# Kernel optimization log

Measured on AMD Instinct MI355X. Metric: run time of the kernel, lower is better.

Reference implementation:

```python
import jax, jax.numpy as jnp
import numpy as np
import math

T_STEPS = 100      # diffusion steps
TED = 16           # time_embed_dim
NODE_C = 4         # node_num_classes
EDGE_C = 2         # edge_num_classes
HID = 64           # hidden_dim
H = 4              # nhead
B = 256            # graphs per batch
NPG = 64           # nodes per graph
DEG = 8            # avg out-degree
N = B * NPG
E = N * DEG
IN_CH = NODE_C + TED  # 20


def sinusoidal_embedding(t_vec, dim):
    # t_vec: [1] float. Matches get_sinusoidal_embedding for even dim.
    half = dim // 2
    scale = math.log(10000.0) / (half - 1)
    freqs = jnp.exp(-jnp.arange(half, dtype=jnp.float32) * scale)  # [half]
    emb = t_vec[:, None] * freqs[None, :]                          # [1, half]
    return jnp.concatenate([jnp.sin(emb), jnp.cos(emb)], axis=1)   # [1, dim]


def transformer_conv(x, src, dst, Wq, bq, Wk, bk, Wv, bv, Ws, bs):
    # PyG TransformerConv, concat=False (mean over heads), root_weight=True,
    # beta=False, no edge features, dropout=0 (eval).
    n = x.shape[0]
    q = (x @ Wq + bq).reshape(n, H, HID)
    k = (x @ Wk + bk).reshape(n, H, HID)
    v = (x @ Wv + bv).reshape(n, H, HID)
    # attention logits per edge, softmax over incoming edges of each dst node
    logits = jnp.sum(q[dst] * k[src], axis=-1) / math.sqrt(HID)    # [E, H]
    lmax = jax.ops.segment_max(logits, dst, num_segments=n)       # [n, H]
    ex = jnp.exp(logits - lmax[dst])                              # [E, H]
    denom = jax.ops.segment_sum(ex, dst, num_segments=n)          # [n, H]
    attn = ex / jnp.where(denom == 0, 1.0, denom)[dst]            # [E, H]
    msg = v[src] * attn[:, :, None]                               # [E, H, HID]
    agg = jax.ops.segment_sum(msg, dst, num_segments=n)           # [n, H, HID]
    return agg.mean(axis=1) + x @ Ws + bs                         # [n, HID]


def setup_inputs() -> dict:
    key = jax.random.key(0)
    ks = jax.random.split(key, 32)

    # node features: random one-hot labels
    labels = jax.random.randint(ks[0], (N,), 0, NODE_C)
    x = jax.nn.one_hot(labels, NODE_C, dtype=jnp.float32)

    # per-graph random edges (kept within each graph via offsets)
    src_l = jax.random.randint(ks[1], (B, NPG * DEG), 0, NPG)
    dst_l = jax.random.randint(ks[2], (B, NPG * DEG), 0, NPG)
    off = (jnp.arange(B) * NPG)[:, None]
    edge_index = jnp.stack([(src_l + off).reshape(-1), (dst_l + off).reshape(-1)]).astype(jnp.int64)

    batch = jnp.repeat(jnp.arange(B, dtype=jnp.int64), NPG)

    def lin(k, fin, fout):
        kw, kb = jax.random.split(k)
        W = jax.random.normal(kw, (fin, fout), jnp.float32) / math.sqrt(fin)
        b = jax.random.normal(kb, (fout,), jnp.float32) * 0.01
        return W, b

    W_time, b_time = lin(ks[3], TED, TED)
    Wq1, bq1 = lin(ks[4], IN_CH, H * HID)
    Wk1, bk1 = lin(ks[5], IN_CH, H * HID)
    Wv1, bv1 = lin(ks[6], IN_CH, H * HID)
    Ws1, bs1 = lin(ks[7], IN_CH, HID)
    Wq2, bq2 = lin(ks[8], HID, H * HID)
    Wk2, bk2 = lin(ks[9], HID, H * HID)
    Wv2, bv2 = lin(ks[10], HID, H * HID)
    Ws2, bs2 = lin(ks[11], HID, HID)
    W_node, b_node = lin(ks[12], HID, NODE_C)
    W_e1, b_e1 = lin(ks[13], 2 * HID, HID)
    W_e2, b_e2 = lin(ks[14], HID, EDGE_C)

    return dict(x=x, edge_index=edge_index, batch=batch, t=50,
                W_time=W_time, b_time=b_time,
                Wq1=Wq1, bq1=bq1, Wk1=Wk1, bk1=bk1, Wv1=Wv1, bv1=bv1, Ws1=Ws1, bs1=bs1,
                Wq2=Wq2, bq2=bq2, Wk2=Wk2, bk2=bk2, Wv2=Wv2, bv2=bv2, Ws2=Ws2, bs2=bs2,
                W_node=W_node, b_node=b_node, W_e1=W_e1, b_e1=b_e1, W_e2=W_e2, b_e2=b_e2)


def reference(x, edge_index, batch, t,
              W_time, b_time,
              Wq1, bq1, Wk1, bk1, Wv1, bv1, Ws1, bs1,
              Wq2, bq2, Wk2, bk2, Wv2, bv2, Ws2, bs2,
              W_node, b_node, W_e1, b_e1, W_e2, b_e2):
    src, dst = edge_index[0], edge_index[1]

    # time embedding: sinusoidal(t/T) -> Linear -> broadcast to all nodes
    t_vec = jnp.asarray([t], jnp.float32) / T_STEPS
    temb = sinusoidal_embedding(t_vec, TED) @ W_time + b_time      # [1, TED]
    temb = jnp.broadcast_to(temb, (x.shape[0], TED))
    x_in = jnp.concatenate([x, temb], axis=1)                      # [N, 20]

    h = jax.nn.relu(transformer_conv(x_in, src, dst, Wq1, bq1, Wk1, bk1, Wv1, bv1, Ws1, bs1))
    h = jax.nn.relu(transformer_conv(h, src, dst, Wq2, bq2, Wk2, bk2, Wv2, bv2, Ws2, bs2))

    node_logits = h @ W_node + b_node                              # [N, 4]

    # to_dense_batch with equal-sized graphs == reshape; vectorized edge MLP
    hd = h.reshape(B, NPG, HID)
    pair = jnp.concatenate([
        jnp.broadcast_to(hd[:, :, None, :], (B, NPG, NPG, HID)),
        jnp.broadcast_to(hd[:, None, :, :], (B, NPG, NPG, HID)),
    ], axis=-1)                                                    # [B, n, n, 2*HID]
    e_hidden = jax.nn.relu(pair @ W_e1 + b_e1)
    edge_logits = e_hidden @ W_e2 + b_e2                           # [B, n, n, 2]
    return node_logits, edge_logits
```

## Files before the change

kernel.cpp:

```cpp
#include <hip/hip_runtime.h>
#include <math.h>

constexpr int EPG  = 512;
constexpr int ETOT = 131072;

constexpr size_t TAB_Q  = 0;
constexpr size_t TAB_K  = 1024;
constexpr size_t TAB_V  = 2048;
constexpr size_t TAB_S  = 3072;
constexpr size_t TAB_LG = 3328;
constexpr size_t OFF_H2P = 65536;

constexpr int PK_V_HI   = 0;
constexpr int PK_V_LO   = 16384;
constexpr int PK_S_HI   = 32768;
constexpr int PK_S_LO   = 36864;
constexpr int PK_E1T_HI = 40960;
constexpr int PK_E1T_LO = 45056;
constexpr int PK_E1B_HI = 49152;
constexpr int PK_E1B_LO = 53248;
constexpr int PK_M_HI   = 57344;
constexpr int PK_M_LO   = 73728;
constexpr int PK_VV_HI  = 90112;
constexpr int PK_VV_LO  = 91136;
constexpr int PK_N_HI   = 92160;
constexpr int PK_N_LO   = 93184;

typedef short bf16x8 __attribute__((ext_vector_type(8)));
typedef float f32x4  __attribute__((ext_vector_type(4)));

__device__ __forceinline__ short f2bf(float x) {
    unsigned u = __float_as_uint(x);
    u = (u + 0x7fffu + ((u >> 16) & 1u)) >> 16;
    return (short)u;
}
__device__ __forceinline__ float bf2f(short h) {
    return __uint_as_float(((unsigned)(unsigned short)h) << 16);
}
__device__ __forceinline__ void splt(float x, short& hi, short& lo) {
    hi = f2bf(x);
    lo = f2bf(x - bf2f(hi));
}
__device__ __forceinline__ unsigned packsplt(float x) {
    short hi, lo; splt(x, hi, lo);
    return ((unsigned)(unsigned short)hi << 16) | (unsigned short)lo;
}

__device__ __forceinline__ f32x4 mfma3(bf16x8 ah, bf16x8 al, bf16x8 bh, bf16x8 bl, f32x4 c) {
    c = __builtin_amdgcn_mfma_f32_16x16x32_bf16(ah, bh, c, 0, 0, 0);
    c = __builtin_amdgcn_mfma_f32_16x16x32_bf16(ah, bl, c, 0, 0, 0);
    c = __builtin_amdgcn_mfma_f32_16x16x32_bf16(al, bh, c, 0, 0, 0);
    return c;
}

__device__ __forceinline__ bf16x8 ldsfrag(const short* p, int rowb, int kb, int lane) {
    return *(const bf16x8*)&p[(rowb + (lane & 15)) * 72 + kb + ((lane >> 4) << 3)];
}
__device__ __forceinline__ bf16x8 gpfrag(const short* p, int colb, int kb, int lane) {
    return *(const bf16x8*)&p[((colb + (lane & 15)) << 6) + kb + ((lane >> 4) << 3)];
}
__device__ __forceinline__ void unpack8(const unsigned* p, bf16x8& hv, bf16x8& lv) {
    uint4 a = *(const uint4*)p;
    uint4 b = *(const uint4*)(p + 4);
    unsigned u[8] = {a.x, a.y, a.z, a.w, b.x, b.y, b.z, b.w};
    bf16x8 h, l;
    #pragma unroll
    for (int i = 0; i < 8; i++) { h[i] = (short)(u[i] >> 16); l[i] = (short)(u[i] & 0xffffu); }
    hv = h; lv = l;
}

__global__ __launch_bounds__(256) void k_tabprep(
    const int* __restrict__ t_ptr,
    const float* __restrict__ Wt,  const float* __restrict__ bt,
    const float* __restrict__ Wq1, const float* __restrict__ bq1,
    const float* __restrict__ Wk1, const float* __restrict__ bk1,
    const float* __restrict__ Wv1, const float* __restrict__ bv1,
    const float* __restrict__ Ws1, const float* __restrict__ bs1,
    const float* __restrict__ Wq2, const float* __restrict__ bq2,
    const float* __restrict__ Wk2, const float* __restrict__ Wv2,
    const float* __restrict__ Ws2, const float* __restrict__ We1,
    const float* __restrict__ Wn,
    float* __restrict__ ws, short* __restrict__ wsh)
{
    const int t = threadIdx.x, b = blockIdx.x;
    if (b < 112) {
        const float* src; int N; int dhi; int nb;
        if (b < 64)      { src = Wv2;           N = 256; dhi = PK_V_HI;   nb = b; }
        else if (b < 80) { src = Ws2;           N = 64;  dhi = PK_S_HI;   nb = b - 64; }
        else if (b < 96) { src = We1;           N = 64;  dhi = PK_E1T_HI; nb = b - 80; }
        else             { src = We1 + 64 * 64; N = 64;  dhi = PK_E1B_HI; nb = b - 96; }
        int dlo = dhi + N * 64;
        int n = nb * 4 + (t >> 6), kk = t & 63;
        float v = src[(size_t)kk * N + n];
        short hi, lo; splt(v, hi, lo);
        wsh[dhi + n * 64 + kk] = hi;
        wsh[dlo + n * 64 + kk] = lo;
        return;
    }
    if (b < 128) {
        int h = (b - 112) >> 2, m0 = ((b - 112) & 3) * 16;
        __shared__ __align__(16) float wq[64][68];
        __shared__ __align__(16) float wk[16][68];
        for (int i = t; i < 1024; i += 256) {
            int r = i >> 4, c4 = (i & 15) * 4;
            *(float4*)&wq[r][c4] = *(const float4*)&Wq2[(size_t)r * 256 + h * 64 + c4];
        }
        {
            int r = t >> 4, c4 = (t & 15) * 4;
            *(float4*)&wk[r][c4] = *(const float4*)&Wk2[(size_t)(m0 + r) * 256 + h * 64 + c4];
        }
        __syncthreads();
        const int m = m0 + (t >> 4), kk0 = (t & 15) * 4;
        const float* wkr = &wk[t >> 4][0];
        for (int kk = kk0; kk < kk0 + 4; kk++) {
            const float* wqr = &wq[kk][0];
            float acc = 0.f;
            #pragma unroll
            for (int a = 0; a < 64; a += 4) {
                float4 qa = *(const float4*)(wqr + a);
                float4 ka = *(const float4*)(wkr + a);
                acc += qa.x * ka.x + qa.y * ka.y + qa.z * ka.z + qa.w * ka.w;
            }
            acc *= 0.125f;
            short hi, lo; splt(acc, hi, lo);
            wsh[PK_M_HI + h * 4096 + m * 64 + kk] = hi;
            wsh[PK_M_LO + h * 4096 + m * 64 + kk] = lo;
        }
        return;
    }
    if (b < 132) {
        int h = b - 128;
        if (t < 64) {
            float acc = 0.f;
            for (int a = 0; a < 64; a++)
                acc += Wk2[(size_t)t * 256 + h * 64 + a] * bq2[h * 64 + a];
            short hi, lo; splt(0.125f * acc, hi, lo);
            wsh[PK_VV_HI + h * 64 + t] = hi;
            wsh[PK_VV_LO + h * 64 + t] = lo;
        }
        return;
    }
    __shared__ float se[16], temb[16];
    __shared__ float q1t[4][256], k1t[4][256], v1t[4][256], s1t[4][64];
    if (t < 8) {
        float tv = (float)(*t_ptr) * 0.01f;
        float scale = logf(10000.0f) / 7.0f;
        float e = tv * expf(-(float)t * scale);
        se[t]     = sinf(e);
        se[t + 8] = cosf(e);
    }
    __syncthreads();
    if (t < 16) {
        float acc = bt[t];
        for (int i = 0; i < 16; i++) acc += se[i] * Wt[i * 16 + t];
        temb[t] = acc;
    }
    __syncthreads();
    {
        const int o = t;
        float tq = 0.f, tk = 0.f, tv = 0.f;
        for (int d = 0; d < 16; d++) {
            float td = temb[d];
            tq += td * Wq1[(4 + d) * 256 + o];
            tk += td * Wk1[(4 + d) * 256 + o];
            tv += td * Wv1[(4 + d) * 256 + o];
        }
        for (int c = 0; c < 4; c++) {
            q1t[c][o] = Wq1[c * 256 + o] + tq + bq1[o];
            k1t[c][o] = Wk1[c * 256 + o] + tk + bk1[o];
            v1t[c][o] = Wv1[c * 256 + o] + tv + bv1[o];
        }
        if (o < 64) {
            float ts = 0.f;
            for (int d = 0; d < 16; d++) ts += temb[d] * Ws1[(4 + d) * 64 + o];
            for (int c = 0; c < 4; c++) s1t[c][o] = Ws1[c * 64 + o] + ts + bs1[o];
        }
    }
    __syncthreads();
    for (int idx = t; idx < 1024; idx += 256) {
        int c = idx >> 8, o = idx & 255;
        ws[TAB_Q + idx] = q1t[c][o];
        ws[TAB_K + idx] = k1t[c][o];
        ws[TAB_V + idx] = v1t[c][o];
    }
    ws[TAB_S + t] = s1t[t >> 6][t & 63];
    if (t < 64) {
        int cd = t >> 4, cs = (t >> 2) & 3, h = t & 3;
        float acc = 0.f;
        for (int d = 0; d < 64; d++) acc += q1t[cd][h * 64 + d] * k1t[cs][h * 64 + d];
        ws[TAB_LG + t] = acc * 0.125f;
    }
    for (int idx = t; idx < 1024; idx += 256) {
        int c = idx >> 6, k = idx & 63;
        float v = (c < 4) ? Wn[k * 4 + c] : 0.f;
        short hi, lo; splt(v, hi, lo);
        wsh[PK_N_HI + idx] = hi;
        wsh[PK_N_LO + idx] = lo;
    }
    for (int idx = 256 + t; idx < 1024; idx += 256) {
        wsh[PK_VV_HI + idx] = 0;
        wsh[PK_VV_LO + idx] = 0;
    }
}

__global__ __launch_bounds__(256) void k_main(
    const float* __restrict__ x, const int* __restrict__ ei,
    const float* __restrict__ ws, const short* __restrict__ wsh,
    const float* __restrict__ bv, const float* __restrict__ bsk,
    unsigned* __restrict__ h2p)
{
    __shared__ __align__(16) char smem[77376];
    short* hHi = (short*)(smem);
    short* hLo = (short*)(smem + 9216);
    short* tHi = (short*)(smem + 18432);
    short* tLo = (short*)(smem + 27648);
    char*  R1base = smem + 36864;
    char*  R2base = smem + 55296;
    char*  Cc     = smem + 73728;
    float* wcolb  = (float*)(smem + 74816);
    float* lgs    = (float*)(smem + 75840);
    int*   cls    = (int*)(smem + 76096);
    int*   cnt4   = (int*)(smem + 76352);
    float* v1t    = (float*)(smem + 36864);
    float* s1t    = (float*)(smem + 40960);

    const int g    = blockIdx.x >> 2;
    const int i0   = (blockIdx.x & 3) * 16;
    const int t    = threadIdx.x;
    const int lane = t & 63, w = t >> 6;
    const int lg4  = ((lane >> 4) << 2);
    const int lg8  = ((lane >> 4) << 3);
    const int l15  = lane & 15;

    short* GHi = (short*)(R1base + w * 4608);
    short* GLo = (short*)(R1base + w * 4608 + 2304);
    float* Sf  = (float*)(R2base + w * 4608);

    for (int i = t; i < 1024; i += 256) v1t[i] = ws[TAB_V + i];
    s1t[t] = ws[TAB_S + t];
    if (t < 64)  lgs[t] = ws[TAB_LG + t];
    if (t < 64) {
        const float* xr = x + (size_t)(g * 64 + t) * 4;
        int c = 0;
        if (xr[1] > 0.5f) c = 1;
        if (xr[2] > 0.5f) c = 2;
        if (xr[3] > 0.5f) c = 3;
        cls[t] = c;
    }
    cnt4[t] = 0;
    for (int i = t; i < 272; i += 256) ((int*)Cc)[i] = 0;
    __syncthreads();

    for (int e = t; e < EPG; e += 256) {
        int ge = g * EPG + e;
        int ls = ei[ge] - g * 64;
        int ld = ei[ETOT + ge] - g * 64;
        atomicAdd(&cnt4[ld * 4 + cls[ls]], 1);
        int lr = ld - i0;
        if ((unsigned)lr < 16u) {
            int idx = lr * 68 + ls;
            atomicAdd((int*)(Cc + (idx & ~3)), 1 << ((idx & 3) * 8));
        }
    }
    __syncthreads();

    {
        const int row = t >> 2, d0 = (t & 3) * 16;
        int cd = cls[row];
        int c0 = cnt4[row * 4], c1 = cnt4[row * 4 + 1],
            c2 = cnt4[row * 4 + 2], c3 = cnt4[row * 4 + 3];
        float a[16];
        #pragma unroll
        for (int hh = 0; hh < 4; hh++) {
            float l0 = lgs[cd * 16 + hh], l1 = lgs[cd * 16 + 4 + hh],
                  l2 = lgs[cd * 16 + 8 + hh], l3 = lgs[cd * 16 + 12 + hh];
            float m = -1e30f;
            if (c0 > 0) m = fmaxf(m, l0);
            if (c1 > 0) m = fmaxf(m, l1);
            if (c2 > 0) m = fmaxf(m, l2);
            if (c3 > 0) m = fmaxf(m, l3);
            float e0 = (c0 > 0) ? (float)c0 * __expf(l0 - m) : 0.f;
            float e1 = (c1 > 0) ? (float)c1 * __expf(l1 - m) : 0.f;
            float e2 = (c2 > 0) ? (float)c2 * __expf(l2 - m) : 0.f;
            float e3 = (c3 > 0) ? (float)c3 * __expf(l3 - m) : 0.f;
            float den = e0 + e1 + e2 + e3;
            float inv = (den > 0.f) ? 0.25f / den : 0.f;
            a[hh * 4 + 0] = e0 * inv; a[hh * 4 + 1] = e1 * inv;
            a[hh * 4 + 2] = e2 * inv; a[hh * 4 + 3] = e3 * inv;
        }
        bf16x8 vh0, vl0, vh1, vl1;
        #pragma unroll
        for (int jj = 0; jj < 16; jj++) {
            int d = d0 + jj;
            float acc = s1t[cd * 64 + d];
            #pragma unroll
            for (int hh = 0; hh < 4; hh++)
                #pragma unroll
                for (int c = 0; c < 4; c++)
                    acc += a[hh * 4 + c] * v1t[c * 256 + hh * 64 + d];
            float o = fmaxf(acc, 0.f);
            short hi, lo; splt(o, hi, lo);
            if (jj < 8) { vh0[jj] = hi; vl0[jj] = lo; }
            else        { vh1[jj - 8] = hi; vl1[jj - 8] = lo; }
            tHi[d * 72 + row] = hi;
            tLo[d * 72 + row] = lo;
        }
        *(bf16x8*)&hHi[row * 72 + d0]     = vh0;
        *(bf16x8*)&hLo[row * 72 + d0]     = vl0;
        *(bf16x8*)&hHi[row * 72 + d0 + 8] = vh1;
        *(bf16x8*)&hLo[row * 72 + d0 + 8] = vl1;
    }
    __syncthreads();

    const int h = w;

    bf16x8 AhQ0 = ldsfrag(hHi, i0, 0, lane),  AhQ1 = ldsfrag(hHi, i0, 32, lane);
    bf16x8 AlQ0 = ldsfrag(hLo, i0, 0, lane),  AlQ1 = ldsfrag(hLo, i0, 32, lane);

    f32x4 skacc = {0.f, 0.f, 0.f, 0.f};
    {
        int cb = w * 16;
        skacc = mfma3(AhQ0, AlQ0, gpfrag(wsh + PK_S_HI, cb, 0, lane),
                                   gpfrag(wsh + PK_S_LO, cb, 0, lane), skacc);
        skacc = mfma3(AhQ1, AlQ1, gpfrag(wsh + PK_S_HI, cb, 32, lane),
                                   gpfrag(wsh + PK_S_LO, cb, 32, lane), skacc);
        float bb = bsk[cb + l15];
        #pragma unroll
        for (int r = 0; r < 4; r++) skacc[r] += bb;
    }

    {
        bf16x8 vv0h = gpfrag(wsh + PK_VV_HI, 0, 0, lane);
        bf16x8 vv0l = gpfrag(wsh + PK_VV_LO, 0, 0, lane);
        bf16x8 vv1h = gpfrag(wsh + PK_VV_HI, 0, 32, lane);
        bf16x8 vv1l = gpfrag(wsh + PK_VV_LO, 0, 32, lane);
        #pragma unroll
        for (int jb = 0; jb < 64; jb += 16) {
            f32x4 wc = {0.f, 0.f, 0.f, 0.f};
            wc = mfma3(ldsfrag(hHi, jb, 0, lane),  ldsfrag(hLo, jb, 0, lane),  vv0h, vv0l, wc);
            wc = mfma3(ldsfrag(hHi, jb, 32, lane), ldsfrag(hLo, jb, 32, lane), vv1h, vv1l, wc);
            if (l15 == h) {
                #pragma unroll
                for (int r = 0; r < 4; r++) wcolb[h * 64 + jb + lg4 + r] = wc[r];
            }
        }
    }

    {
        const short* pmh = wsh + PK_M_HI + h * 4096;
        const short* pml = wsh + PK_M_LO + h * 4096;
        #pragma unroll
        for (int mb = 0; mb < 64; mb += 16) {
            f32x4 ga = {0.f, 0.f, 0.f, 0.f};
            ga = mfma3(AhQ0, AlQ0, gpfrag(pmh, mb, 0, lane),  gpfrag(pml, mb, 0, lane),  ga);
            ga = mfma3(AhQ1, AlQ1, gpfrag(pmh, mb, 32, lane), gpfrag(pml, mb, 32, lane), ga);
            #pragma unroll
            for (int r = 0; r < 4; r++) {
                short hi, lo; splt(ga[r], hi, lo);
                GHi[(lg4 + r) * 72 + mb + l15] = hi;
                GLo[(lg4 + r) * 72 + mb + l15] = lo;
            }
        }
    }

    {
        bf16x8 g0h = ldsfrag(GHi, 0, 0, lane),  g0l = ldsfrag(GLo, 0, 0, lane);
        bf16x8 g1h = ldsfrag(GHi, 0, 32, lane), g1l = ldsfrag(GLo, 0, 32, lane);
        #pragma unroll
        for (int jb = 0; jb < 64; jb += 16) {
            f32x4 s = {0.f, 0.f, 0.f, 0.f};
            s = mfma3(g0h, g0l, ldsfrag(hHi, jb, 0, lane),  ldsfrag(hLo, jb, 0, lane),  s);
            s = mfma3(g1h, g1l, ldsfrag(hHi, jb, 32, lane), ldsfrag(hLo, jb, 32, lane), s);
            #pragma unroll
            for (int r = 0; r < 4; r++)
                Sf[(lg4 + r) * 68 + jb + l15] = s[r];
        }
    }

    bf16x8 pa0h, pa0l, pa1h, pa1l;
    {
        const int lr = l15;
        float sv[16];
        {
            const float* sp = Sf + lr * 68;
            float4 a0 = *(const float4*)(sp + lg8);
            float4 a1 = *(const float4*)(sp + lg8 + 4);
            float4 a2 = *(const float4*)(sp + 32 + lg8);
            float4 a3 = *(const float4*)(sp + 32 + lg8 + 4);
            sv[0]=a0.x; sv[1]=a0.y; sv[2]=a0.z; sv[3]=a0.w;
            sv[4]=a1.x; sv[5]=a1.y; sv[6]=a1.z; sv[7]=a1.w;
            sv[8]=a2.x; sv[9]=a2.y; sv[10]=a2.z; sv[11]=a2.w;
            sv[12]=a3.x; sv[13]=a3.y; sv[14]=a3.z; sv[15]=a3.w;
        }
        int cv[16];
        {
            const unsigned* crow = (const unsigned*)(Cc + lr * 68);
            unsigned c0 = crow[lg8 >> 2], c1 = crow[(lg8 >> 2) + 1];
            unsigned c2 = crow[(32 + lg8) >> 2], c3 = crow[((32 + lg8) >> 2) + 1];
            #pragma unroll
            for (int e = 0; e < 4; e++) {
                cv[e]      = (c0 >> (e * 8)) & 255;
                cv[4 + e]  = (c1 >> (e * 8)) & 255;
                cv[8 + e]  = (c2 >> (e * 8)) & 255;
                cv[12 + e] = (c3 >> (e * 8)) & 255;
            }
        }
        #pragma unroll
        for (int e = 0; e < 8; e++) {
            sv[e]     += wcolb[h * 64 + lg8 + e];
            sv[8 + e] += wcolb[h * 64 + 32 + lg8 + e];
        }
        float m = -1e30f;
        #pragma unroll
        for (int e = 0; e < 16; e++) if (cv[e] > 0) m = fmaxf(m, sv[e]);
        m = fmaxf(m, __shfl_xor(m, 16));
        m = fmaxf(m, __shfl_xor(m, 32));
        float den = 0.f; float p[16];
        #pragma unroll
        for (int e = 0; e < 16; e++) {
            p[e] = (cv[e] > 0) ? (float)cv[e] * __expf(sv[e] - m) : 0.f;
            den += p[e];
        }
        den += __shfl_xor(den, 16);
        den += __shfl_xor(den, 32);
        float inv = (den > 0.f) ? 1.f / den : 0.f;
        #pragma unroll
        for (int e = 0; e < 8; e++) {
            short hi, lo;
            splt(p[e] * inv, hi, lo);      pa0h[e] = hi; pa0l[e] = lo;
            splt(p[8 + e] * inv, hi, lo);  pa1h[e] = hi; pa1l[e] = lo;
        }
    }

    #pragma unroll
    for (int fb = 0; fb < 64; fb += 16) {
        f32x4 u = {0.f, 0.f, 0.f, 0.f};
        u = mfma3(pa0h, pa0l, ldsfrag(tHi, fb, 0, lane),  ldsfrag(tLo, fb, 0, lane),  u);
        u = mfma3(pa1h, pa1l, ldsfrag(tHi, fb, 32, lane), ldsfrag(tLo, fb, 32, lane), u);
        #pragma unroll
        for (int r = 0; r < 4; r++) {
            short hi, lo; splt(u[r], hi, lo);
            GHi[(lg4 + r) * 72 + fb + l15] = hi;
            GLo[(lg4 + r) * 72 + fb + l15] = lo;
        }
    }

    {
        bf16x8 u0h = ldsfrag(GHi, 0, 0, lane),  u0l = ldsfrag(GLo, 0, 0, lane);
        bf16x8 u1h = ldsfrag(GHi, 0, 32, lane), u1l = ldsfrag(GLo, 0, 32, lane);
        #pragma unroll
        for (int db = 0; db < 64; db += 16) {
            int gc = h * 64 + db;
            f32x4 pv = {0.f, 0.f, 0.f, 0.f};
            pv = mfma3(u0h, u0l, gpfrag(wsh + PK_V_HI, gc, 0, lane),
                                  gpfrag(wsh + PK_V_LO, gc, 0, lane), pv);
            pv = mfma3(u1h, u1l, gpfrag(wsh + PK_V_HI, gc, 32, lane),
                                  gpfrag(wsh + PK_V_LO, gc, 32, lane), pv);
            #pragma unroll
            for (int r = 0; r < 4; r++)
                Sf[(lg4 + r) * 68 + db + l15] = pv[r];
        }
    }
    __syncthreads();

    {
        const int d = w * 16 + l15;
        float bvsum = bv[d] + bv[64 + d] + bv[128 + d] + bv[192 + d];
        #pragma unroll
        for (int r = 0; r < 4; r++) {
            float sum = 0.f;
            #pragma unroll
            for (int hh = 0; hh < 4; hh++)
                sum += ((const float*)(R2base + hh * 4608))[(lg4 + r) * 68 + d];
            float v = fmaxf(0.25f * (sum + bvsum) + skacc[r], 0.f);
            h2p[(size_t)(g * 64 + i0 + lg4 + r) * 64 + d] = packsplt(v);
        }
    }
}

__global__ __launch_bounds__(256) void k_edge(
    const short* __restrict__ wsh, const unsigned* __restrict__ h2g,
    const float* __restrict__ bn, const float* __restrict__ be1,
    const float* __restrict__ We2, const float* __restrict__ be2,
    float* __restrict__ out)
{
    __shared__ __align__(16) char smem[39680];
    unsigned* h2P = (unsigned*)(smem);
    float*    Af  = (float*)(smem + 17408);
    float*    BTf = (float*)(smem + 21760);
    float*    w2s = (float*)(smem + 39168);

    const int g  = blockIdx.x >> 2;
    const int i0 = (blockIdx.x & 3) * 16;
    const int t  = threadIdx.x;
    const int lane = t & 63, w = t >> 6;
    const int lg4 = ((lane >> 4) << 2);
    const int lg8 = ((lane >> 4) << 3);
    const int l15 = lane & 15;

    {
        int row = t >> 2, c16 = (t & 3) * 16;
        const unsigned* src = h2g + (size_t)(g * 64 + row) * 64 + c16;
        #pragma unroll
        for (int q = 0; q < 4; q++)
            *(uint4*)&h2P[row * 68 + c16 + q * 4] = *(const uint4*)(src + q * 4);
    }
    if (t < 128) w2s[(t & 1) * 64 + (t >> 1)] = We2[t];
    __syncthreads();

    {
        bf16x8 aq0, lq0, aq1, lq1;
        const unsigned* ap = h2P + (i0 + l15) * 68;
        unpack8(ap + lg8, aq0, lq0);
        unpack8(ap + 32 + lg8, aq1, lq1);
        {
            int colb = w * 16;
            bf16x8 e0h = gpfrag(wsh + PK_E1T_HI, colb, 0, lane),  e0l = gpfrag(wsh + PK_E1T_LO, colb, 0, lane);
            bf16x8 e1h = gpfrag(wsh + PK_E1T_HI, colb, 32, lane), e1l = gpfrag(wsh + PK_E1T_LO, colb, 32, lane);
            f32x4 aa = {0.f, 0.f, 0.f, 0.f};
            aa = mfma3(aq0, lq0, e0h, e0l, aa);
            aa = mfma3(aq1, lq1, e1h, e1l, aa);
            float bev = be1[colb + l15];
            #pragma unroll
            for (int r = 0; r < 4; r++)
                Af[(lg4 + r) * 68 + colb + l15] = aa[r] + bev;
        }
        if (w == 0) {
            bf16x8 n0h = gpfrag(wsh + PK_N_HI, 0, 0, lane),  n0l = gpfrag(wsh + PK_N_LO, 0, 0, lane);
            bf16x8 n1h = gpfrag(wsh + PK_N_HI, 0, 32, lane), n1l = gpfrag(wsh + PK_N_LO, 0, 32, lane);
            f32x4 nl = {0.f, 0.f, 0.f, 0.f};
            nl = mfma3(aq0, lq0, n0h, n0l, nl);
            nl = mfma3(aq1, lq1, n1h, n1l, nl);
            if (l15 < 4) {
                #pragma unroll
                for (int r = 0; r < 4; r++)
                    out[(size_t)(g * 64 + i0 + lg4 + r) * 4 + l15] = nl[r] + bn[l15];
            }
        }
    }
    {
        bf16x8 af0, lf0, af1, lf1;
        const unsigned* ap = h2P + (w * 16 + l15) * 68;
        unpack8(ap + lg8, af0, lf0);
        unpack8(ap + 32 + lg8, af1, lf1);
        #pragma unroll
        for (int ct = 0; ct < 4; ct++) {
            int colb = ct * 16;
            bf16x8 b0h = gpfrag(wsh + PK_E1B_HI, colb, 0, lane),  b0l = gpfrag(wsh + PK_E1B_LO, colb, 0, lane);
            bf16x8 b1h = gpfrag(wsh + PK_E1B_HI, colb, 32, lane), b1l = gpfrag(wsh + PK_E1B_LO, colb, 32, lane);
            f32x4 bb = {0.f, 0.f, 0.f, 0.f};
            bb = mfma3(af0, lf0, b0h, b0l, bb);
            bb = mfma3(af1, lf1, b1h, b1l, bb);
            #pragma unroll
            for (int r = 0; r < 4; r++)
                BTf[(colb + l15) * 68 + w * 16 + lg4 + r] = bb[r];
        }
    }
    __syncthreads();

    {
        const int j = t & 63;
        float e0[4], e1[4];
        const float cb0 = be2[0], cb1 = be2[1];
        #pragma unroll
        for (int ii = 0; ii < 4; ii++) { e0[ii] = cb0; e1[ii] = cb1; }
        for (int kb = 0; kb < 4; kb++) {
            const int k0 = kb * 16;
            float bj[16], wa[16], wb[16];
            #pragma unroll
            for (int q = 0; q < 16; q++) {
                bj[q] = BTf[(k0 + q) * 68 + j];
                wa[q] = w2s[k0 + q];
                wb[q] = w2s[64 + k0 + q];
            }
            #pragma unroll
            for (int ii = 0; ii < 4; ii++) {
                const float* ar = &Af[(w * 4 + ii) * 68 + k0];
                #pragma unroll
                for (int q = 0; q < 16; q += 4) {
                    float4 a4 = *(const float4*)(ar + q);
                    float s;
                    s = fmaxf(a4.x + bj[q + 0], 0.f); e0[ii] += s * wa[q + 0]; e1[ii] += s * wb[q + 0];
                    s = fmaxf(a4.y + bj[q + 1], 0.f); e0[ii] += s * wa[q + 1]; e1[ii] += s * wb[q + 1];
                    s = fmaxf(a4.z + bj[q + 2], 0.f); e0[ii] += s * wa[q + 2]; e1[ii] += s * wb[q + 2];
                    s = fmaxf(a4.w + bj[q + 3], 0.f); e0[ii] += s * wa[q + 3]; e1[ii] += s * wb[q + 3];
                }
            }
        }
        float2* oe = (float2*)(out + 65536);
        #pragma unroll
        for (int ii = 0; ii < 4; ii++)
            oe[(size_t)(g * 64 + i0 + w * 4 + ii) * 64 + j] = make_float2(e0[ii], e1[ii]);
    }
}

extern "C" void kernel_launch(void* const* d_in, const int* in_sizes, int n_in,
                              void* d_out, int out_size, void* d_ws, size_t ws_size,
                              hipStream_t stream)
{
    const float* x    = (const float*)d_in[0];
    const int*   ei   = (const int*)d_in[1];
    const int*   tptr = (const int*)d_in[3];
    const float* Wt   = (const float*)d_in[4];
    const float* bt   = (const float*)d_in[5];
    const float* Wq1  = (const float*)d_in[6];
    const float* bq1  = (const float*)d_in[7];
    const float* Wk1  = (const float*)d_in[8];
    const float* bk1  = (const float*)d_in[9];
    const float* Wv1  = (const float*)d_in[10];
    const float* bv1  = (const float*)d_in[11];
    const float* Ws1  = (const float*)d_in[12];
    const float* bs1  = (const float*)d_in[13];
    const float* Wq2  = (const float*)d_in[14];
    const float* bq2  = (const float*)d_in[15];
    const float* Wk2  = (const float*)d_in[16];
    const float* Wv2  = (const float*)d_in[18];
    const float* bv2  = (const float*)d_in[19];
    const float* Ws2  = (const float*)d_in[20];
    const float* bs2  = (const float*)d_in[21];
    const float* Wn   = (const float*)d_in[22];
    const float* bn   = (const float*)d_in[23];
    const float* We1  = (const float*)d_in[24];
    const float* be1  = (const float*)d_in[25];
    const float* We2  = (const float*)d_in[26];
    const float* be2  = (const float*)d_in[27];

    float* ws  = (float*)d_ws;
    short* wsh = (short*)(ws + 4096);
    unsigned* h2p = (unsigned*)(ws + OFF_H2P);
    float* out = (float*)d_out;

    k_tabprep<<<133, 256, 0, stream>>>(tptr, Wt, bt, Wq1, bq1, Wk1, bk1, Wv1, bv1,
                                       Ws1, bs1, Wq2, bq2, Wk2, Wv2, Ws2, We1, Wn,
                                       ws, wsh);
    k_main<<<1024, 256, 0, stream>>>(x, ei, ws, wsh, bv2, bs2, h2p);
    k_edge<<<1024, 256, 0, stream>>>(wsh, h2p, bn, be1, We2, be2, out);
}
```

Measured before the change: 64.02 us.

## Split layer-1 computation into separate kernel to avoid 4x redundant recompute

Layer-1 node features, their transposed copy and the per-head column term were previously recomputed by each of the four blocks handling a graph. A new k_h1 kernel (one block per graph) now computes them once and writes packed hi/lo bf16 pairs to global memory. k_main reads those fragments from global memory instead of LDS, which shrinks its shared-memory footprint and can raise occupancy. The cost is an extra kernel launch plus global round-trips for h1, its transpose and wcol, and MFMA operands are now unpacked from global loads.

```diff
diff --git a/kernel.cpp b/kernel.cpp
--- a/kernel.cpp
+++ b/kernel.cpp
@@ -9,7 +9,10 @@
 constexpr size_t TAB_V  = 2048;
 constexpr size_t TAB_S  = 3072;
 constexpr size_t TAB_LG = 3328;
-constexpr size_t OFF_H2P = 65536;
+constexpr size_t OFF_H2P  = 65536;
+constexpr size_t OFF_H1P  = 1114112;
+constexpr size_t OFF_H1TP = 2162688;
+constexpr size_t OFF_WCOL = 3211264;
 
 constexpr int PK_V_HI   = 0;
 constexpr int PK_V_LO   = 16384;
@@ -53,9 +56,6 @@
     return c;
 }
 
-__device__ __forceinline__ bf16x8 ldsfrag(const short* p, int rowb, int kb, int lane) {
-    return *(const bf16x8*)&p[(rowb + (lane & 15)) * 72 + kb + ((lane >> 4) << 3)];
-}
 __device__ __forceinline__ bf16x8 gpfrag(const short* p, int colb, int kb, int lane) {
     return *(const bf16x8*)&p[((colb + (lane & 15)) << 6) + kb + ((lane >> 4) << 3)];
 }
@@ -67,6 +67,10 @@
     #pragma unroll
     for (int i = 0; i < 8; i++) { h[i] = (short)(u[i] >> 16); l[i] = (short)(u[i] & 0xffffu); }
     hv = h; lv = l;
+}
+__device__ __forceinline__ void pkfrag(const unsigned* p, int rowb, int kb, int stride,
+                                       int lane, bf16x8& hv, bf16x8& lv) {
+    unpack8(p + (size_t)(rowb + (lane & 15)) * stride + kb + ((lane >> 4) << 3), hv, lv);
 }
 
 __global__ __launch_bounds__(256) void k_tabprep(
@@ -203,42 +207,25 @@
     }
 }
 
-__global__ __launch_bounds__(256) void k_main(
+__global__ __launch_bounds__(256) void k_h1(
     const float* __restrict__ x, const int* __restrict__ ei,
     const float* __restrict__ ws, const short* __restrict__ wsh,
-    const float* __restrict__ bv, const float* __restrict__ bsk,
-    unsigned* __restrict__ h2p)
+    unsigned* __restrict__ h1p, unsigned* __restrict__ h1tp,
+    float* __restrict__ wcolg)
 {
-    __shared__ __align__(16) char smem[77376];
-    short* hHi = (short*)(smem);
-    short* hLo = (short*)(smem + 9216);
-    short* tHi = (short*)(smem + 18432);
-    short* tLo = (short*)(smem + 27648);
-    char*  R1base = smem + 36864;
-    char*  R2base = smem + 55296;
-    char*  Cc     = smem + 73728;
-    float* wcolb  = (float*)(smem + 74816);
-    float* lgs    = (float*)(smem + 75840);
-    int*   cls    = (int*)(smem + 76096);
-    int*   cnt4   = (int*)(smem + 76352);
-    float* v1t    = (float*)(smem + 36864);
-    float* s1t    = (float*)(smem + 40960);
-
-    const int g    = blockIdx.x >> 2;
-    const int i0   = (blockIdx.x & 3) * 16;
-    const int t    = threadIdx.x;
-    const int lane = t & 63, w = t >> 6;
-    const int lg4  = ((lane >> 4) << 2);
-    const int lg8  = ((lane >> 4) << 3);
-    const int l15  = lane & 15;
-
-    short* GHi = (short*)(R1base + w * 4608);
-    short* GLo = (short*)(R1base + w * 4608 + 2304);
-    float* Sf  = (float*)(R2base + w * 4608);
+    __shared__ float v1t[1024];
+    __shared__ float s1t[256];
+    __shared__ float lgs[64];
+    __shared__ float vvf[256];
+    __shared__ int   cls[64];
+    __shared__ int   cnt4[256];
+
+    const int g = blockIdx.x, t = threadIdx.x;
 
     for (int i = t; i < 1024; i += 256) v1t[i] = ws[TAB_V + i];
     s1t[t] = ws[TAB_S + t];
-    if (t < 64)  lgs[t] = ws[TAB_LG + t];
+    if (t < 64) lgs[t] = ws[TAB_LG + t];
+    vvf[t] = bf2f(wsh[PK_VV_HI + t]) + bf2f(wsh[PK_VV_LO + t]);
     if (t < 64) {
         const float* xr = x + (size_t)(g * 64 + t) * 4;
         int c = 0;
@@ -248,7 +235,6 @@
         cls[t] = c;
     }
     cnt4[t] = 0;
-    for (int i = t; i < 272; i += 256) ((int*)Cc)[i] = 0;
     __syncthreads();
 
     for (int e = t; e < EPG; e += 256) {
@@ -256,11 +242,6 @@
         int ls = ei[ge] - g * 64;
         int ld = ei[ETOT + ge] - g * 64;
         atomicAdd(&cnt4[ld * 4 + cls[ls]], 1);
-        int lr = ld - i0;
-        if ((unsigned)lr < 16u) {
-            int idx = lr * 68 + ls;
-            atomicAdd((int*)(Cc + (idx & ~3)), 1 << ((idx & 3) * 8));
-        }
     }
     __syncthreads();
 
@@ -288,7 +269,8 @@
             a[hh * 4 + 0] = e0 * inv; a[hh * 4 + 1] = e1 * inv;
             a[hh * 4 + 2] = e2 * inv; a[hh * 4 + 3] = e3 * inv;
         }
-        bf16x8 vh0, vl0, vh1, vl1;
+        float h1v[16];
+        unsigned pk[16];
         #pragma unroll
         for (int jj = 0; jj < 16; jj++) {
             int d = d0 + jj;
@@ -299,23 +281,81 @@
                 for (int c = 0; c < 4; c++)
                     acc += a[hh * 4 + c] * v1t[c * 256 + hh * 64 + d];
             float o = fmaxf(acc, 0.f);
-            short hi, lo; splt(o, hi, lo);
-            if (jj < 8) { vh0[jj] = hi; vl0[jj] = lo; }
-            else        { vh1[jj - 8] = hi; vl1[jj - 8] = lo; }
-            tHi[d * 72 + row] = hi;
-            tLo[d * 72 + row] = lo;
-        }
-        *(bf16x8*)&hHi[row * 72 + d0]     = vh0;
-        *(bf16x8*)&hLo[row * 72 + d0]     = vl0;
-        *(bf16x8*)&hHi[row * 72 + d0 + 8] = vh1;
-        *(bf16x8*)&hLo[row * 72 + d0 + 8] = vl1;
-    }
-    __syncthreads();
-
-    const int h = w;
-
-    bf16x8 AhQ0 = ldsfrag(hHi, i0, 0, lane),  AhQ1 = ldsfrag(hHi, i0, 32, lane);
-    bf16x8 AlQ0 = ldsfrag(hLo, i0, 0, lane),  AlQ1 = ldsfrag(hLo, i0, 32, lane);
+            h1v[jj] = o;
+            pk[jj] = packsplt(o);
+        }
+        unsigned* dst = h1p + ((size_t)(g * 64 + row) << 6) + d0;
+        *(uint4*)(dst)      = make_uint4(pk[0], pk[1], pk[2], pk[3]);
+        *(uint4*)(dst + 4)  = make_uint4(pk[4], pk[5], pk[6], pk[7]);
+        *(uint4*)(dst + 8)  = make_uint4(pk[8], pk[9], pk[10], pk[11]);
+        *(uint4*)(dst + 12) = make_uint4(pk[12], pk[13], pk[14], pk[15]);
+        unsigned* tb = h1tp + (size_t)g * 4096;
+        #pragma unroll
+        for (int jj = 0; jj < 16; jj++) tb[(d0 + jj) * 64 + row] = pk[jj];
+        float ph[4];
+        #pragma unroll
+        for (int hh = 0; hh < 4; hh++) {
+            float acc = 0.f;
+            #pragma unroll
+            for (int jj = 0; jj < 16; jj++) acc += h1v[jj] * vvf[hh * 64 + d0 + jj];
+            ph[hh] = acc;
+        }
+        #pragma unroll
+        for (int hh = 0; hh < 4; hh++) {
+            ph[hh] += __shfl_xor(ph[hh], 1);
+            ph[hh] += __shfl_xor(ph[hh], 2);
+        }
+        int hsel = t & 3;
+        wcolg[(size_t)g * 256 + hsel * 64 + row] = ph[hsel];
+    }
+}
+
+__global__ __launch_bounds__(256) void k_main(
+    const int* __restrict__ ei, const short* __restrict__ wsh,
+    const unsigned* __restrict__ h1p, const unsigned* __restrict__ h1tp,
+    const float* __restrict__ wcolg,
+    const float* __restrict__ bv, const float* __restrict__ bsk,
+    unsigned* __restrict__ h2p)
+{
+    __shared__ __align__(16) char smem[36928];
+    char*  R1 = smem;
+    char*  R2 = smem + 17408;
+    char*  Cc = smem + 34816;
+    float* wcolS = (float*)(smem + 35904);
+
+    const int g    = blockIdx.x >> 2;
+    const int i0   = (blockIdx.x & 3) * 16;
+    const int t    = threadIdx.x;
+    const int lane = t & 63, w = t >> 6;
+    const int lg4  = ((lane >> 4) << 2);
+    const int lg8  = ((lane >> 4) << 3);
+    const int l15  = lane & 15;
+    const int h    = w;
+
+    unsigned* Gp  = (unsigned*)(R1 + w * 4352);
+    float*    Sf  = (float*)(R2 + w * 4352);
+    unsigned* Up  = (unsigned*)(R2 + w * 4352);
+
+    wcolS[t] = wcolg[(size_t)g * 256 + t];
+    for (int i = t; i < 272; i += 256) ((int*)Cc)[i] = 0;
+    __syncthreads();
+
+    for (int e = t; e < EPG; e += 256) {
+        int ge = g * EPG + e;
+        int ls = ei[ge] - g * 64;
+        int ld = ei[ETOT + ge] - g * 64;
+        int lr = ld - i0;
+        if ((unsigned)lr < 16u) {
+            int idx = lr * 68 + ls;
+            atomicAdd((int*)(Cc + (idx & ~3)), 1 << ((idx & 3) * 8));
+        }
+    }
+    __syncthreads();
+
+    const unsigned* h1g = h1p + ((size_t)g << 12);
+    bf16x8 AhQ0, AlQ0, AhQ1, AlQ1;
+    pkfrag(h1g, i0, 0, 64, lane, AhQ0, AlQ0);
+    pkfrag(h1g, i0, 32, 64, lane, AhQ1, AlQ1);
 
     f32x4 skacc = {0.f, 0.f, 0.f, 0.f};
     {
@@ -330,23 +370,6 @@
     }
 
     {
-        bf16x8 vv0h = gpfrag(wsh + PK_VV_HI, 0, 0, lane);
-        bf16x8 vv0l = gpfrag(wsh + PK_VV_LO, 0, 0, lane);
-        bf16x8 vv1h = gpfrag(wsh + PK_VV_HI, 0, 32, lane);
-        bf16x8 vv1l = gpfrag(wsh + PK_VV_LO, 0, 32, lane);
-        #pragma unroll
-        for (int jb = 0; jb < 64; jb += 16) {
-            f32x4 wc = {0.f, 0.f, 0.f, 0.f};
-            wc = mfma3(ldsfrag(hHi, jb, 0, lane),  ldsfrag(hLo, jb, 0, lane),  vv0h, vv0l, wc);
-            wc = mfma3(ldsfrag(hHi, jb, 32, lane), ldsfrag(hLo, jb, 32, lane), vv1h, vv1l, wc);
-            if (l15 == h) {
-                #pragma unroll
-                for (int r = 0; r < 4; r++) wcolb[h * 64 + jb + lg4 + r] = wc[r];
-            }
-        }
-    }
-
-    {
         const short* pmh = wsh + PK_M_HI + h * 4096;
         const short* pml = wsh + PK_M_LO + h * 4096;
         #pragma unroll
@@ -355,29 +378,29 @@
             ga = mfma3(AhQ0, AlQ0, gpfrag(pmh, mb, 0, lane),  gpfrag(pml, mb, 0, lane),  ga);
             ga = mfma3(AhQ1, AlQ1, gpfrag(pmh, mb, 32, lane), gpfrag(pml, mb, 32, lane), ga);
             #pragma unroll
-            for (int r = 0; r < 4; r++) {
-                short hi, lo; splt(ga[r], hi, lo);
-                GHi[(lg4 + r) * 72 + mb + l15] = hi;
-                GLo[(lg4 + r) * 72 + mb + l15] = lo;
-            }
-        }
-    }
-
-    {
-        bf16x8 g0h = ldsfrag(GHi, 0, 0, lane),  g0l = ldsfrag(GLo, 0, 0, lane);
-        bf16x8 g1h = ldsfrag(GHi, 0, 32, lane), g1l = ldsfrag(GLo, 0, 32, lane);
+            for (int r = 0; r < 4; r++)
+                Gp[(lg4 + r) * 68 + mb + l15] = packsplt(ga[r]);
+        }
+    }
+
+    {
+        bf16x8 g0h, g0l, g1h, g1l;
+        pkfrag(Gp, 0, 0, 68, lane, g0h, g0l);
+        pkfrag(Gp, 0, 32, 68, lane, g1h, g1l);
         #pragma unroll
         for (int jb = 0; jb < 64; jb += 16) {
+            bf16x8 b0h, b0l, b1h, b1l;
+            pkfrag(h1g, jb, 0, 64, lane, b0h, b0l);
+            pkfrag(h1g, jb, 32, 64, lane, b1h, b1l);
             f32x4 s = {0.f, 0.f, 0.f, 0.f};
-            s = mfma3(g0h, g0l, ldsfrag(hHi, jb, 0, lane),  ldsfrag(hLo, jb, 0, lane),  s);
-            s = mfma3(g1h, g1l, ldsfrag(hHi, jb, 32, lane), ldsfrag(hLo, jb, 32, lane), s);
+            s = mfma3(g0h, g0l, b0h, b0l, s);
+            s = mfma3(g1h, g1l, b1h, b1l, s);
             #pragma unroll
             for (int r = 0; r < 4; r++)
                 Sf[(lg4 + r) * 68 + jb + l15] = s[r];
         }
     }
 
-    bf16x8 pa0h, pa0l, pa1h, pa1l;
     {
         const int lr = l15;
         float sv[16];
@@ -407,8 +430,8 @@
         }
         #pragma unroll
         for (int e = 0; e < 8; e++) {
-            sv[e]     += wcolb[h * 64 + lg8 + e];
-            sv[8 + e] += wcolb[h * 64 + 32 + lg8 + e];
+            sv[e]     += wcolS[h * 64 + lg8 + e];
+            sv[8 + e] += wcolS[h * 64 + 32 + lg8 + e];
         }
         float m = -1e30f;
         #pragma unroll
@@ -424,30 +447,40 @@
         den += __shfl_xor(den, 16);
         den += __shfl_xor(den, 32);
         float inv = (den > 0.f) ? 1.f / den : 0.f;
-        #pragma unroll
-        for (int e = 0; e < 8; e++) {
-            short hi, lo;
-            splt(p[e] * inv, hi, lo);      pa0h[e] = hi; pa0l[e] = lo;
-            splt(p[8 + e] * inv, hi, lo);  pa1h[e] = hi; pa1l[e] = lo;
-        }
-    }
-
-    #pragma unroll
-    for (int fb = 0; fb < 64; fb += 16) {
-        f32x4 u = {0.f, 0.f, 0.f, 0.f};
-        u = mfma3(pa0h, pa0l, ldsfrag(tHi, fb, 0, lane),  ldsfrag(tLo, fb, 0, lane),  u);
-        u = mfma3(pa1h, pa1l, ldsfrag(tHi, fb, 32, lane), ldsfrag(tLo, fb, 32, lane), u);
-        #pragma unroll
-        for (int r = 0; r < 4; r++) {
-            short hi, lo; splt(u[r], hi, lo);
-            GHi[(lg4 + r) * 72 + fb + l15] = hi;
-            GLo[(lg4 + r) * 72 + fb + l15] = lo;
-        }
-    }
-
-    {
-        bf16x8 u0h = ldsfrag(GHi, 0, 0, lane),  u0l = ldsfrag(GLo, 0, 0, lane);
-        bf16x8 u1h = ldsfrag(GHi, 0, 32, lane), u1l = ldsfrag(GLo, 0, 32, lane);
+        unsigned pk[16];
+        #pragma unroll
+        for (int e = 0; e < 16; e++) pk[e] = packsplt(p[e] * inv);
+        unsigned* pp = Gp + lr * 68;
+        *(uint4*)(pp + lg8)          = make_uint4(pk[0], pk[1], pk[2], pk[3]);
+        *(uint4*)(pp + lg8 + 4)      = make_uint4(pk[4], pk[5], pk[6], pk[7]);
+        *(uint4*)(pp + 32 + lg8)     = make_uint4(pk[8], pk[9], pk[10], pk[11]);
+        *(uint4*)(pp + 32 + lg8 + 4) = make_uint4(pk[12], pk[13], pk[14], pk[15]);
+    }
+
+    {
+        bf16x8 p0h, p0l, p1h, p1l;
+        pkfrag(Gp, 0, 0, 68, lane, p0h, p0l);
+        pkfrag(Gp, 0, 32, 68, lane, p1h, p1l);
+        const unsigned* tg = h1tp + ((size_t)g << 12);
+        #pragma unroll
+        for (int fb = 0; fb < 64; fb += 16) {
+            bf16x8 b0h, b0l, b1h, b1l;
+            pkfrag(tg, fb, 0, 64, lane, b0h, b0l);
+            pkfrag(tg, fb, 32, 64, lane, b1h, b1l);
+            f32x4 u = {0.f, 0.f, 0.f, 0.f};
+            u = mfma3(p0h, p0l, b0h, b0l, u);
+            u = mfma3(p1h, p1l, b1h, b1l, u);
+            #pragma unroll
+            for (int r = 0; r < 4; r++)
+                Up[(lg4 + r) * 68 + fb + l15] = packsplt(u[r]);
+        }
+    }
+
+    {
+        bf16x8 u0h, u0l, u1h, u1l;
+        pkfrag(Up, 0, 0, 68, lane, u0h, u0l);
+        pkfrag(Up, 0, 32, 68, lane, u1h, u1l);
+        float* PVf = (float*)Gp;
         #pragma unroll
         for (int db = 0; db < 64; db += 16) {
             int gc = h * 64 + db;
@@ -458,7 +491,7 @@
                                   gpfrag(wsh + PK_V_LO, gc, 32, lane), pv);
             #pragma unroll
             for (int r = 0; r < 4; r++)
-                Sf[(lg4 + r) * 68 + db + l15] = pv[r];
+                PVf[(lg4 + r) * 68 + db + l15] = pv[r];
         }
     }
     __syncthreads();
@@ -471,7 +504,7 @@
             float sum = 0.f;
             #pragma unroll
             for (int hh = 0; hh < 4; hh++)
-                sum += ((const float*)(R2base + hh * 4608))[(lg4 + r) * 68 + d];
+                sum += ((const float*)(R1 + hh * 4352))[(lg4 + r) * 68 + d];
             float v = fmaxf(0.25f * (sum + bvsum) + skacc[r], 0.f);
             h2p[(size_t)(g * 64 + i0 + lg4 + r) * 64 + d] = packsplt(v);
         }
@@ -627,12 +660,16 @@
 
     float* ws  = (float*)d_ws;
     short* wsh = (short*)(ws + 4096);
-    unsigned* h2p = (unsigned*)(ws + OFF_H2P);
+    unsigned* h2p  = (unsigned*)(ws + OFF_H2P);
+    unsigned* h1p  = (unsigned*)(ws + OFF_H1P);
+    unsigned* h1tp = (unsigned*)(ws + OFF_H1TP);
+    float*    wcolg = ws + OFF_WCOL;
     float* out = (float*)d_out;
 
     k_tabprep<<<133, 256, 0, stream>>>(tptr, Wt, bt, Wq1, bq1, Wk1, bk1, Wv1, bv1,
                                        Ws1, bs1, Wq2, bq2, Wk2, Wv2, Ws2, We1, Wn,
                                        ws, wsh);
-    k_main<<<1024, 256, 0, stream>>>(x, ei, ws, wsh, bv2, bs2, h2p);
+    k_h1<<<256, 256, 0, stream>>>(x, ei, ws, wsh, h1p, h1tp, wcolg);
+    k_main<<<1024, 256, 0, stream>>>(ei, wsh, h1p, h1tp, wcolg, bv2, bs2, h2p);
     k_edge<<<1024, 256, 0, stream>>>(wsh, h2p, bn, be1, We2, be2, out);
 }
```

Result: slower. 78.70 us (+22.9%).
